# Performance work log

Hardware: AMD Instinct MI355X
Metric: run time of the kernel (lower is better)

Reference implementation:

```python
import jax, jax.numpy as jnp
import numpy as np

N, D, F, K = 50000, 256, 256, 10


def setup_inputs() -> dict:
    key = jax.random.key(0)
    k1, k2, k3, k4, k5, k6 = jax.random.split(key, 6)
    # neighbor indices in [-1, N); -1 marks padding (masked out in forward)
    return {
        "Z1": jax.random.normal(k1, (N, D), dtype=jnp.float32),
        "Z2": jax.random.normal(k2, (N, D), dtype=jnp.float32),
        "Wr": jax.random.normal(k3, (D, F), dtype=jnp.float32),
        "Wnr": jax.random.normal(k4, (D, F), dtype=jnp.float32),
        "n1": jax.random.randint(k5, (N, K), -1, N, dtype=jnp.int64),
        "n2": jax.random.randint(k6, (N, K), -1, N, dtype=jnp.int64),
    }


def _protein(Z, nb, Wr, Wnr):
    residues_signal = Z @ Wr                      # [N, F]
    neighbors_base_signal = Z @ Wnr               # [N, F]
    mask = (nb > -1)                              # [N, K]
    # index -1 wraps to last row (as in torch), then is zeroed by the mask
    feats = neighbors_base_signal[nb] * mask[..., None].astype(Z.dtype)  # [N, K, F]
    norm = jnp.maximum(mask.sum(axis=1), 1).astype(Z.dtype)[:, None]     # [N, 1]
    neighbors_signal = feats.sum(axis=1) / norm
    return jax.nn.relu(residues_signal + neighbors_signal)


def reference(Z1, Z2, Wr, Wnr, n1, n2):
    out1 = _protein(Z1, n1, Wr, Wnr)
    out2 = _protein(Z2, n2, Wr, Wnr)
    return jnp.stack([out1, out2])  # [2, N, F]
```

## Files before the change

kernel.cpp:

```cpp
#include <hip/hip_runtime.h>
#include <hip/hip_bf16.h>
#include <hip/hip_fp8.h>

#define NNODE 50000
#define MTOT  100000
#define NF    256
#define KNB   10

typedef unsigned short u16;
typedef float f32x4 __attribute__((ext_vector_type(4)));
typedef float f32x2 __attribute__((ext_vector_type(2)));
typedef short bf16x8 __attribute__((ext_vector_type(8)));

__device__ __forceinline__ u16 f2bf(float f) {
    unsigned u = __builtin_bit_cast(unsigned, f);
    unsigned r = (u + 0x7fffu + ((u >> 16) & 1u)) >> 16;
    return (u16)r;
}
__device__ __forceinline__ unsigned char f2f8(float f) {
    return (unsigned char)__hip_fp8_e4m3(f).__x;
}
__device__ __forceinline__ float f8tof(unsigned char b) {
    __hip_fp8_e4m3 h;
    h.__x = (__hip_fp8_storage_t)b;
    return (float)h;
}
template <int WORD>
__device__ __forceinline__ f32x2 cvt2_fp8(unsigned v) {
#if __has_builtin(__builtin_amdgcn_cvt_pk_f32_fp8)
    auto c = __builtin_amdgcn_cvt_pk_f32_fp8((int)v, WORD);
    f32x2 r; r.x = c[0]; r.y = c[1];
    return r;
#else
    unsigned s = WORD ? (v >> 16) : v;
    f32x2 r;
    r.x = f8tof((unsigned char)(s & 0xff));
    r.y = f8tof((unsigned char)((s >> 8) & 0xff));
    return r;
#endif
}
template <int WORD>
__device__ __forceinline__ unsigned pk_fp8(float a, float b, unsigned old) {
#if __has_builtin(__builtin_amdgcn_cvt_pk_fp8_f32)
    return (unsigned)__builtin_amdgcn_cvt_pk_fp8_f32(a, b, (int)old, WORD);
#else
    unsigned lo = (unsigned)f2f8(a) | ((unsigned)f2f8(b) << 8);
    return WORD ? ((old & 0x0000ffffu) | (lo << 16)) : ((old & 0xffff0000u) | lo);
#endif
}
__device__ __forceinline__ void gload_lds16(const void* g, void* l) {
    __builtin_amdgcn_global_load_lds(
        (const __attribute__((address_space(1))) unsigned int*)g,
        (__attribute__((address_space(3))) unsigned int*)l, 16, 0, 0);
}

__global__ __launch_bounds__(256) void cast_all(const float* __restrict__ Z1,
                                                const float* __restrict__ Z2,
                                                const float* __restrict__ Wr,
                                                const float* __restrict__ Wnr,
                                                u16* __restrict__ Zleft,
                                                unsigned char* __restrict__ Z8,
                                                u16* __restrict__ WT,
                                                unsigned char* __restrict__ WT8) {
    int b = blockIdx.x;
    if (b < 12500) {
        unsigned id = b * 256 + threadIdx.x;
        int m = id >> 5;
        int d = (id & 31) << 3;
        const float* src = (m < NNODE) ? (Z1 + (size_t)m * 256 + d)
                                       : (Z2 + (size_t)(m - NNODE) * 256 + d);
        float4 a = *(const float4*)src;
        float4 bb = *(const float4*)(src + 4);
        uint4 o;
        o.x = (unsigned)f2bf(a.x) | ((unsigned)f2bf(a.y) << 16);
        o.y = (unsigned)f2bf(a.z) | ((unsigned)f2bf(a.w) << 16);
        o.z = (unsigned)f2bf(bb.x) | ((unsigned)f2bf(bb.y) << 16);
        o.w = (unsigned)f2bf(bb.z) | ((unsigned)f2bf(bb.w) << 16);
        *(uint4*)(Zleft + (size_t)m * 256 + d) = o;
        uint2 o8;
        o8.x = (unsigned)f2f8(a.x) | ((unsigned)f2f8(a.y) << 8) |
               ((unsigned)f2f8(a.z) << 16) | ((unsigned)f2f8(a.w) << 24);
        o8.y = (unsigned)f2f8(bb.x) | ((unsigned)f2f8(bb.y) << 8) |
               ((unsigned)f2f8(bb.z) << 16) | ((unsigned)f2f8(bb.w) << 24);
        *(uint2*)(Z8 + (size_t)m * 256 + d) = o8;
    } else if (b < 12756) {
        int id = (b - 12500) * 256 + threadIdx.x;
        int n = id >> 8, k = id & 255;
        WT[n * 256 + k] = f2bf(Wr[(size_t)k * 256 + n]);
    } else {
        int id = (b - 12756) * 256 + threadIdx.x;
        int n = id >> 8, k = id & 255;
        int kb = k ^ (((n >> 2) & 1) << 3);
        WT8[n * 256 + kb] = f2f8(Wnr[(size_t)k * 256 + n]);
    }
}

__device__ __forceinline__ void stageA(const u16* __restrict__ Zl, u16* dst,
                                       int m0, int kt, int t) {
    int row = t >> 3, gd = t & 7;
    int gs = gd ^ (row & 7);
    int grow = m0 + row;
    if (grow >= MTOT) grow = MTOT - 1;
    gload_lds16(Zl + (size_t)grow * 256 + kt + gs * 8, dst + t * 8);
}
__device__ __forceinline__ void stageBl(const u16* __restrict__ WT, u16* dst,
                                        int kt, int t) {
    #pragma unroll
    for (int rp = 0; rp < 4; ++rp) {
        int c = rp * 512 + t;
        int col = c >> 3, gd = c & 7;
        int gs = gd ^ (col & 7);
        gload_lds16(WT + (size_t)col * 256 + kt + gs * 8, dst + c * 8);
    }
}
__device__ __forceinline__ void stageBr(const unsigned char* __restrict__ WT8,
                                        unsigned char* dst, int ktr, int t) {
    #pragma unroll
    for (int rp = 0; rp < 2; ++rp) {
        int c = rp * 512 + t;
        int col = c >> 2, gd = c & 3;
        int gs = gd ^ (col & 3);
        gload_lds16(WT8 + (size_t)col * 256 + ktr + gs * 16, dst + c * 16);
    }
}

__device__ __forceinline__ void mfma_left(const u16* sAc, const u16* sBc, int lane,
                                          int wr, int wc, f32x4 (&acc)[2][4]) {
    const int hi = lane >> 4, l15 = lane & 15;
    #pragma unroll
    for (int kk = 0; kk < 64; kk += 32) {
        int g = (kk >> 3) + hi;
        bf16x8 af[2], bfr[4];
        #pragma unroll
        for (int i = 0; i < 2; ++i) {
            int row = wr * 32 + i * 16 + l15;
            af[i] = *(const bf16x8*)((const char*)sAc + row * 128 + ((g ^ (row & 7)) << 4));
        }
        #pragma unroll
        for (int j = 0; j < 4; ++j) {
            int col = wc * 64 + j * 16 + l15;
            bfr[j] = *(const bf16x8*)((const char*)sBc + col * 128 + ((g ^ (col & 7)) << 4));
        }
        #pragma unroll
        for (int i = 0; i < 2; ++i)
            #pragma unroll
            for (int j = 0; j < 4; ++j)
                acc[i][j] = __builtin_amdgcn_mfma_f32_16x16x32_bf16(af[i], bfr[j], acc[i][j], 0, 0, 0);
    }
}
__device__ __forceinline__ void mfma_right(const unsigned char* sZ, const unsigned char* sBc,
                                           int R, int lane, int wr, int wc,
                                           f32x4 (&acc)[2][4]) {
    const int hi = lane >> 4, l15 = lane & 15;
    #pragma unroll
    for (int m = 0; m < 2; ++m) {
        long long az[2], bz[4];
        #pragma unroll
        for (int i = 0; i < 2; ++i) {
            int row = wr * 32 + i * 16 + l15;
            int g8 = R * 8 + m * 4 + hi;
            az[i] = *(const long long*)(sZ + row * 256 + ((g8 ^ (row & 7)) << 3));
        }
        #pragma unroll
        for (int j = 0; j < 4; ++j) {
            int col = wc * 64 + j * 16 + l15;
            int G = 2 * m + (hi >> 1);
            int hb = ((hi & 1) ^ ((col >> 2) & 1)) << 3;
            bz[j] = *(const long long*)(sBc + col * 64 + ((G ^ (col & 3)) << 4) + hb);
        }
        #pragma unroll
        for (int i = 0; i < 2; ++i)
            #pragma unroll
            for (int j = 0; j < 4; ++j)
                acc[i][j] = __builtin_amdgcn_mfma_f32_16x16x32_fp8_fp8(az[i], bz[j], acc[i][j], 0, 0, 0);
    }
}

__device__ __forceinline__ void consume(const uint2 (&gv)[KNB], unsigned mask, int cnt,
                                        int w, int lane, int s, unsigned char* sZ) {
    f32x2 a0 = {0.f, 0.f}, a1 = {0.f, 0.f}, a2 = {0.f, 0.f}, a3 = {0.f, 0.f};
    #pragma unroll
    for (int k = 0; k < KNB; ++k) {
        float mm = (float)((mask >> k) & 1u);
        f32x2 m2 = {mm, mm};
        a0 += m2 * cvt2_fp8<0>(gv[k].x);
        a1 += m2 * cvt2_fp8<1>(gv[k].x);
        a2 += m2 * cvt2_fp8<0>(gv[k].y);
        a3 += m2 * cvt2_fp8<1>(gv[k].y);
    }
    float sc = 1.0f / (float)(cnt > 0 ? cnt : 1);
    unsigned w0 = pk_fp8<0>(a0.x * sc, a0.y * sc, 0u);
    w0 = pk_fp8<1>(a1.x * sc, a1.y * sc, w0);
    unsigned w1 = pk_fp8<0>(a2.x * sc, a2.y * sc, 0u);
    w1 = pk_fp8<1>(a3.x * sc, a3.y * sc, w1);
    int rl = w * 8 + s * 2 + (lane >> 5);
    int gp = (lane & 31) ^ (rl & 7);
    *(uint2*)(sZ + rl * 256 + (gp << 3)) = make_uint2(w0, w1);
}

template <int S>
__device__ __forceinline__ void left_step(const u16* __restrict__ Zl,
                                          const u16* __restrict__ WT,
                                          const unsigned char* __restrict__ Z8,
                                          const int* __restrict__ n1,
                                          const int* __restrict__ n2,
                                          u16* sA0, u16* sA1, u16* sBL, unsigned char* sZ,
                                          int m0, int t, int lane, int w, int wr, int wc,
                                          int2 (&icur)[5], unsigned& pmask, int& pcnt,
                                          uint2 (&gv)[KNB], f32x4 (&acc)[2][4]) {
    u16* sAcur = (S & 1) ? sA1 : sA0;
    u16* sAnxt = (S & 1) ? sA0 : sA1;
    stageBl(WT, sBL, S * 64, t);
    __builtin_amdgcn_sched_barrier(0);
    if (S < 3) stageA(Zl, sAnxt, m0, (S + 1) * 64, t);
    __builtin_amdgcn_sched_barrier(0);
    int2 inxt[5];
    if (S < 3) {
        int rl = w * 8 + (S + 1) * 2 + (lane >> 5);
        int g = m0 + rl;
        if (g >= MTOT) g = MTOT - 1;
        int p = (g >= NNODE);
        const int* nb = (p ? n2 : n1) + (size_t)(g - p * NNODE) * KNB;
        #pragma unroll
        for (int q = 0; q < 5; ++q) inxt[q] = *(const int2*)(nb + 2 * q);
    }
    __builtin_amdgcn_sched_barrier(0);
    if (S > 0) consume(gv, pmask, pcnt, w, lane, S - 1, sZ);
    __builtin_amdgcn_sched_barrier(0);
    {
        int g = m0 + w * 8 + S * 2 + (lane >> 5);
        if (g >= MTOT) g = MTOT - 1;
        int p = (g >= NNODE);
        const unsigned char* zb = Z8 + (size_t)p * ((size_t)NNODE * 256) + ((lane & 31) << 3);
        unsigned mask = 0;
        int cnt = 0;
        #pragma unroll
        for (int k = 0; k < KNB; ++k) {
            int ix = (k & 1) ? icur[k >> 1].y : icur[k >> 1].x;
            int valid = (ix > -1) ? 1 : 0;
            mask |= (unsigned)valid << k;
            cnt += valid;
            gv[k] = *(const uint2*)(zb + (size_t)(valid ? ix : 0) * 256);
        }
        pmask = mask;
        pcnt = cnt;
    }
    if (S < 3) {
        #pragma unroll
        for (int q = 0; q < 5; ++q) icur[q] = inxt[q];
    }
    __builtin_amdgcn_sched_barrier(0);
    if (S < 3) asm volatile("s_waitcnt vmcnt(16)" ::: "memory");
    else       asm volatile("s_waitcnt vmcnt(10)" ::: "memory");
    __builtin_amdgcn_s_barrier();
    __builtin_amdgcn_s_setprio(1);
    mfma_left(sAcur, sBL, lane, wr, wc, acc);
    __builtin_amdgcn_s_setprio(0);
    __builtin_amdgcn_s_barrier();
}

__global__ __launch_bounds__(512, 4) void gemm_fused(const u16* __restrict__ Zl,
                                                     const unsigned char* __restrict__ Z8,
                                                     const u16* __restrict__ WT,
                                                     const unsigned char* __restrict__ WT8,
                                                     const int* __restrict__ n1,
                                                     const int* __restrict__ n2,
                                                     float* __restrict__ C) {
    __shared__ char smem[65536];
    u16* sA0 = (u16*)smem;
    u16* sA1 = (u16*)(smem + 8192);
    u16* sBL = (u16*)(smem + 16384);
    unsigned char* sBr0 = (unsigned char*)(smem + 16384);
    unsigned char* sBr1 = (unsigned char*)(smem + 32768);
    unsigned char* sZ = (unsigned char*)(smem + 49152);

    const int m0 = blockIdx.x * 64;
    const int t = threadIdx.x;
    const int lane = t & 63;
    const int w = t >> 6;
    const int wr = w >> 2, wc = w & 3;

    f32x4 acc[2][4] = {};
    uint2 gv[KNB];
    int2 icur[5];
    unsigned pmask = 0;
    int pcnt = 0;

    stageA(Zl, sA0, m0, 0, t);
    {
        int g = m0 + w * 8 + (lane >> 5);
        if (g >= MTOT) g = MTOT - 1;
        int p = (g >= NNODE);
        const int* nb = (p ? n2 : n1) + (size_t)(g - p * NNODE) * KNB;
        #pragma unroll
        for (int q = 0; q < 5; ++q) icur[q] = *(const int2*)(nb + 2 * q);
    }

    left_step<0>(Zl, WT, Z8, n1, n2, sA0, sA1, sBL, sZ, m0, t, lane, w, wr, wc, icur, pmask, pcnt, gv, acc);
    left_step<1>(Zl, WT, Z8, n1, n2, sA0, sA1, sBL, sZ, m0, t, lane, w, wr, wc, icur, pmask, pcnt, gv, acc);
    left_step<2>(Zl, WT, Z8, n1, n2, sA0, sA1, sBL, sZ, m0, t, lane, w, wr, wc, icur, pmask, pcnt, gv, acc);
    left_step<3>(Zl, WT, Z8, n1, n2, sA0, sA1, sBL, sZ, m0, t, lane, w, wr, wc, icur, pmask, pcnt, gv, acc);

    consume(gv, pmask, pcnt, w, lane, 3, sZ);
    stageBr(WT8, sBr0, 0, t);
    asm volatile("s_waitcnt vmcnt(0)" ::: "memory");
    asm volatile("s_waitcnt lgkmcnt(0)" ::: "memory");
    __builtin_amdgcn_s_barrier();

#define RSTEP(R)                                                            \
    do {                                                                    \
        if ((R) < 3) {                                                      \
            stageBr(WT8, ((R) & 1) ? sBr0 : sBr1, ((R) + 1) * 64, t);       \
            asm volatile("s_waitcnt vmcnt(2)" ::: "memory");                \
        } else {                                                            \
            asm volatile("s_waitcnt vmcnt(0)" ::: "memory");                \
        }                                                                   \
        __builtin_amdgcn_s_barrier();                                       \
        __builtin_amdgcn_s_setprio(1);                                      \
        mfma_right(sZ, ((R) & 1) ? sBr1 : sBr0, (R), lane, wr, wc, acc);    \
        __builtin_amdgcn_s_setprio(0);                                      \
        if ((R) < 3) __builtin_amdgcn_s_barrier();                          \
    } while (0)

    RSTEP(0);
    RSTEP(1);
    RSTEP(2);
    RSTEP(3);
#undef RSTEP

    const int l15 = lane & 15;
    const int hi = lane >> 4;
    #pragma unroll
    for (int i = 0; i < 2; ++i) {
        int rbase = m0 + wr * 32 + i * 16 + (hi << 2);
        #pragma unroll
        for (int j = 0; j < 4; ++j) {
            int col = wc * 64 + j * 16 + l15;
            #pragma unroll
            for (int q = 0; q < 4; ++q) {
                int row = rbase + q;
                if (row < MTOT) C[(size_t)row * NF + col] = fmaxf(acc[i][j][q], 0.f);
            }
        }
    }
}

extern "C" void kernel_launch(void* const* d_in, const int* in_sizes, int n_in,
                              void* d_out, int out_size, void* d_ws, size_t ws_size,
                              hipStream_t stream) {
    const float* Z1  = (const float*)d_in[0];
    const float* Z2  = (const float*)d_in[1];
    const float* Wr  = (const float*)d_in[2];
    const float* Wnr = (const float*)d_in[3];
    const int*   n1  = (const int*)d_in[4];
    const int*   n2  = (const int*)d_in[5];
    float* out = (float*)d_out;

    u16* WT            = (u16*)d_ws;
    unsigned char* WT8 = (unsigned char*)d_ws + 131072;
    u16* Zleft         = (u16*)((unsigned char*)d_ws + 196608);
    unsigned char* Z8  = (unsigned char*)d_ws + 196608 + (size_t)MTOT * 512;

    cast_all<<<13012, 256, 0, stream>>>(Z1, Z2, Wr, Wnr, Zleft, Z8, WT, WT8);
    gemm_fused<<<1563, 512, 0, stream>>>(Zleft, Z8, WT, WT8, n1, n2, out);
}
```

Before: 109.2 us.

## Split neighbor gather across half-waves with 16-byte loads and shuffle reduction

```diff
diff --git a/kernel.cpp b/kernel.cpp
--- a/kernel.cpp
+++ b/kernel.cpp
@@ -176,26 +176,40 @@
     }
 }
 
-__device__ __forceinline__ void consume(const uint2 (&gv)[KNB], unsigned mask, int cnt,
+__device__ __forceinline__ void consume(const uint4 (&gv)[5], unsigned mask, int cnt,
                                         int w, int lane, int s, unsigned char* sZ) {
-    f32x2 a0 = {0.f, 0.f}, a1 = {0.f, 0.f}, a2 = {0.f, 0.f}, a3 = {0.f, 0.f};
-    #pragma unroll
-    for (int k = 0; k < KNB; ++k) {
-        float mm = (float)((mask >> k) & 1u);
+    f32x2 a[8];
+    #pragma unroll
+    for (int j = 0; j < 8; ++j) a[j] = f32x2{0.f, 0.f};
+    #pragma unroll
+    for (int q = 0; q < 5; ++q) {
+        float mm = (float)((mask >> q) & 1u);
         f32x2 m2 = {mm, mm};
-        a0 += m2 * cvt2_fp8<0>(gv[k].x);
-        a1 += m2 * cvt2_fp8<1>(gv[k].x);
-        a2 += m2 * cvt2_fp8<0>(gv[k].y);
-        a3 += m2 * cvt2_fp8<1>(gv[k].y);
-    }
-    float sc = 1.0f / (float)(cnt > 0 ? cnt : 1);
-    unsigned w0 = pk_fp8<0>(a0.x * sc, a0.y * sc, 0u);
-    w0 = pk_fp8<1>(a1.x * sc, a1.y * sc, w0);
-    unsigned w1 = pk_fp8<0>(a2.x * sc, a2.y * sc, 0u);
-    w1 = pk_fp8<1>(a3.x * sc, a3.y * sc, w1);
-    int rl = w * 8 + s * 2 + (lane >> 5);
-    int gp = (lane & 31) ^ (rl & 7);
-    *(uint2*)(sZ + rl * 256 + (gp << 3)) = make_uint2(w0, w1);
+        a[0] += m2 * cvt2_fp8<0>(gv[q].x); a[1] += m2 * cvt2_fp8<1>(gv[q].x);
+        a[2] += m2 * cvt2_fp8<0>(gv[q].y); a[3] += m2 * cvt2_fp8<1>(gv[q].y);
+        a[4] += m2 * cvt2_fp8<0>(gv[q].z); a[5] += m2 * cvt2_fp8<1>(gv[q].z);
+        a[6] += m2 * cvt2_fp8<0>(gv[q].w); a[7] += m2 * cvt2_fp8<1>(gv[q].w);
+    }
+    int cfull = cnt + __shfl_xor(cnt, 32, 64);
+    #pragma unroll
+    for (int j = 0; j < 8; ++j) {
+        a[j].x += __shfl_xor(a[j].x, 32, 64);
+        a[j].y += __shfl_xor(a[j].y, 32, 64);
+    }
+    float sc = 1.0f / (float)(cfull > 0 ? cfull : 1);
+    unsigned pw[4];
+    #pragma unroll
+    for (int j = 0; j < 4; ++j) {
+        unsigned v = pk_fp8<0>(a[2 * j].x * sc, a[2 * j].y * sc, 0u);
+        pw[j] = pk_fp8<1>(a[2 * j + 1].x * sc, a[2 * j + 1].y * sc, v);
+    }
+    if (lane < 32) {
+        int rl = w * 8 + s * 2 + ((lane >> 4) & 1);
+        int m = lane & 15;
+        int e = rl & 7;
+        *(uint2*)(sZ + rl * 256 + ((( 2 * m    ) ^ e) << 3)) = make_uint2(pw[0], pw[1]);
+        *(uint2*)(sZ + rl * 256 + (((2 * m + 1) ^ e) << 3)) = make_uint2(pw[2], pw[3]);
+    }
 }
 
 template <int S>
@@ -207,17 +221,18 @@
                                           u16* sA0, u16* sA1, u16* sBL, unsigned char* sZ,
                                           int m0, int t, int lane, int w, int wr, int wc,
                                           int2 (&icur)[5], unsigned& pmask, int& pcnt,
-                                          uint2 (&gv)[KNB], f32x4 (&acc)[2][4]) {
+                                          uint4 (&gv)[5], f32x4 (&acc)[2][4]) {
     u16* sAcur = (S & 1) ? sA1 : sA0;
     u16* sAnxt = (S & 1) ? sA0 : sA1;
+    const int rowoff = (lane >> 4) & 1;
+    const int ehalf = lane >> 5;
     stageBl(WT, sBL, S * 64, t);
     __builtin_amdgcn_sched_barrier(0);
     if (S < 3) stageA(Zl, sAnxt, m0, (S + 1) * 64, t);
     __builtin_amdgcn_sched_barrier(0);
     int2 inxt[5];
     if (S < 3) {
-        int rl = w * 8 + (S + 1) * 2 + (lane >> 5);
-        int g = m0 + rl;
+        int g = m0 + w * 8 + (S + 1) * 2 + rowoff;
         if (g >= MTOT) g = MTOT - 1;
         int p = (g >= NNODE);
         const int* nb = (p ? n2 : n1) + (size_t)(g - p * NNODE) * KNB;
@@ -228,19 +243,19 @@
     if (S > 0) consume(gv, pmask, pcnt, w, lane, S - 1, sZ);
     __builtin_amdgcn_sched_barrier(0);
     {
-        int g = m0 + w * 8 + S * 2 + (lane >> 5);
+        int g = m0 + w * 8 + S * 2 + rowoff;
         if (g >= MTOT) g = MTOT - 1;
         int p = (g >= NNODE);
-        const unsigned char* zb = Z8 + (size_t)p * ((size_t)NNODE * 256) + ((lane & 31) << 3);
+        const unsigned char* zb = Z8 + (size_t)p * ((size_t)NNODE * 256) + ((lane & 15) << 4);
         unsigned mask = 0;
         int cnt = 0;
         #pragma unroll
-        for (int k = 0; k < KNB; ++k) {
-            int ix = (k & 1) ? icur[k >> 1].y : icur[k >> 1].x;
+        for (int q = 0; q < 5; ++q) {
+            int ix = ehalf ? icur[q].y : icur[q].x;
             int valid = (ix > -1) ? 1 : 0;
-            mask |= (unsigned)valid << k;
+            mask |= (unsigned)valid << q;
             cnt += valid;
-            gv[k] = *(const uint2*)(zb + (size_t)(valid ? ix : 0) * 256);
+            gv[q] = *(const uint4*)(zb + (size_t)(valid ? ix : 0) * 256);
         }
         pmask = mask;
         pcnt = cnt;
@@ -250,8 +265,8 @@
         for (int q = 0; q < 5; ++q) icur[q] = inxt[q];
     }
     __builtin_amdgcn_sched_barrier(0);
-    if (S < 3) asm volatile("s_waitcnt vmcnt(16)" ::: "memory");
-    else       asm volatile("s_waitcnt vmcnt(10)" ::: "memory");
+    if (S < 3) asm volatile("s_waitcnt vmcnt(11)" ::: "memory");
+    else       asm volatile("s_waitcnt vmcnt(5)" ::: "memory");
     __builtin_amdgcn_s_barrier();
     __builtin_amdgcn_s_setprio(1);
     mfma_left(sAcur, sBL, lane, wr, wc, acc);
@@ -281,14 +296,14 @@
     const int wr = w >> 2, wc = w & 3;
 
     f32x4 acc[2][4] = {};
-    uint2 gv[KNB];
+    uint4 gv[5];
     int2 icur[5];
     unsigned pmask = 0;
     int pcnt = 0;
 
     stageA(Zl, sA0, m0, 0, t);
     {
-        int g = m0 + w * 8 + (lane >> 5);
+        int g = m0 + w * 8 + ((lane >> 4) & 1);
         if (g >= MTOT) g = MTOT - 1;
         int p = (g >= NNODE);
         const int* nb = (p ? n2 : n1) + (size_t)(g - p * NNODE) * KNB;
```

Result: slower. 121.9 us (+11.6%).
